# Kernel tuning notes

Hardware: AMD Instinct MI355X
Metric: run time of the kernel (lower is better)

## Reference

```python
import jax, jax.numpy as jnp
import numpy as np

B, C, H, W, D = 4, 8, 160, 160, 160
N_PER = 100000
IMAGE_DIM = 160


def setup_inputs() -> dict:
    key = jax.random.key(0)
    k1, k2 = jax.random.split(key)
    image_features = jax.random.normal(k1, (B, C, H, W, D), dtype=jnp.float32)
    # coords uniform in [0, IMAGE_DIM); last 3 columns are x,y,z
    graph_features = jax.random.uniform(k2, (B * N_PER, 3), dtype=jnp.float32) * IMAGE_DIM
    batch = jnp.arange(B * N_PER, dtype=jnp.int32) // N_PER  # equal count per image (required by cat dim=0)
    return {
        "image_features": image_features,
        "graph_features": graph_features,
        "batch": batch,
        "image_dim": IMAGE_DIM,
    }


def _trilerp(image_features, graph_features, image_dim):
    Bn, Cc, Hh, Ww, Dd = image_features.shape
    n_per = graph_features.shape[0] // Bn
    dt = graph_features.dtype
    factor = jnp.asarray(image_dim, dt) / Hh  # original uses image_dim/h for all axes
    xyz = graph_features[:, -3:].reshape(Bn, n_per, 3) / factor  # [B, n, 3]
    x, y, z = xyz[..., 0], xyz[..., 1], xyz[..., 2]

    def bounds(v, size):
        lo = jnp.minimum(jnp.floor(v), size - 1)
        hi = jnp.minimum(jnp.ceil(v), size - 1)
        return lo, hi

    x1f, x2f = bounds(x, Hh)
    y1f, y2f = bounds(y, Ww)
    z1f, z2f = bounds(z, Dd)
    x1, x2 = x1f.astype(jnp.int32), x2f.astype(jnp.int32)
    y1, y2 = y1f.astype(jnp.int32), y2f.astype(jnp.int32)
    z1, z2 = z1f.astype(jnp.int32), z2f.astype(jnp.int32)
    # weights exactly as in original (degenerate-to-zero when floor==ceil, kept faithfully)
    wx, wx2 = x - x1f, x2f - x
    wy, wy2 = y - y1f, y2f - y
    wz, wz2 = z - z1f, z2f - z

    def per_image(img, x1, x2, y1, y2, z1, z2, wx, wx2, wy, wy2, wz, wz2):
        # img: [C, H, W, D]; indices/weights: [n]
        def g(xi, yi, zi):
            return img[:, xi, yi, zi]  # [C, n]

        def lerp_y(zc):
            lx1 = g(x2, y1, zc) * wx + g(x1, y1, zc) * wx2
            lx2 = g(x2, y2, zc) * wx + g(x1, y2, zc) * wx2
            return lx2 * wy + lx1 * wy2

        return lerp_y(z2) * wz + lerp_y(z1) * wz2  # [C, n]

    out = jax.vmap(per_image)(
        image_features, x1, x2, y1, y2, z1, z2, wx, wx2, wy, wy2, wz, wz2
    )  # [B, C, n]
    # torch.cat over batch along dim 0 of [C, n] blocks == reshape to [B*C, n]; then permute(1,0)
    return out.reshape(Bn * Cc, n_per).T  # [n, B*C]


def reference(image_features, graph_features, batch, image_dim):
    # batch is arange(N)//n_per (sorted, equal counts), so grouping == reshape; batch unused numerically
    return _trilerp(image_features, graph_features, image_dim)
```

## Files before the change

kernel.cpp:

```cpp
#include <hip/hip_runtime.h>
#include <hip/hip_fp16.h>

constexpr int B = 4, C = 8, H = 160, W = 160, Dd = 160, NPER = 100000;
constexpr long HWD = (long)H * W * Dd;
constexpr int  TOTAL_PTS = NPER * B;
constexpr int  TOTAL_OUT = NPER * B * C;
constexpr int  NKEYS = B * H * W;
constexpr int  SCAN_BLOCKS = NKEYS / 256;

typedef float  f32x4 __attribute__((ext_vector_type(4)));

constexpr size_t WS_IMG_BYTES   = (size_t)B * HWD * C * sizeof(__half);
constexpr size_t WS_COUNTS_OFF  = WS_IMG_BYTES;
constexpr size_t WS_PART_OFF    = WS_COUNTS_OFF + (size_t)NKEYS * 4;
constexpr size_t WS_PAY_OFF     = WS_PART_OFF + 4096;
constexpr size_t WS_NEEDED      = WS_PAY_OFF + (size_t)TOTAL_PTS * 16;

__device__ __forceinline__ float load_image_dim(const int* dimp) {
    int iv = dimp[0];
    return (iv > 0 && iv < 1000000) ? (float)iv : __int_as_float(iv);
}

struct Coord {
    int x1, x2, y1, y2, z1, z2;
    float wx, wx2, wy, wy2, wz, wz2;
};
__device__ __forceinline__ Coord coord_from_xyz(float gx, float gy, float gz,
                                                float factor) {
    Coord c;
    float x = gx / factor, y = gy / factor, z = gz / factor;
    float x1f = fminf(floorf(x), (float)(H - 1));
    float x2f = fminf(ceilf(x),  (float)(H - 1));
    float y1f = fminf(floorf(y), (float)(W - 1));
    float y2f = fminf(ceilf(y),  (float)(W - 1));
    float z1f = fminf(floorf(z), (float)(Dd - 1));
    float z2f = fminf(ceilf(z),  (float)(Dd - 1));
    c.x1 = max(0, (int)x1f); c.x2 = max(0, (int)x2f);
    c.y1 = max(0, (int)y1f); c.y2 = max(0, (int)y2f);
    c.z1 = max(0, (int)z1f); c.z2 = max(0, (int)z2f);
    c.wx = x - x1f; c.wx2 = x2f - x;
    c.wy = y - y1f; c.wy2 = y2f - y;
    c.wz = z - z1f; c.wz2 = z2f - z;
    return c;
}

__global__ __launch_bounds__(256) void zero_kernel(int* __restrict__ counts) {
    int i = blockIdx.x * 256 + threadIdx.x;
    if (i < NKEYS) counts[i] = 0;
}

__global__ __launch_bounds__(256) void hist_kernel(
    const float* __restrict__ gf, const int* __restrict__ dimp,
    int* __restrict__ counts)
{
    int p = blockIdx.x * 256 + threadIdx.x;
    if (p >= TOTAL_PTS) return;
    float factor = load_image_dim(dimp) / (float)H;
    int b = p / NPER;
    Coord c = coord_from_xyz(gf[(long)p*3], gf[(long)p*3+1], gf[(long)p*3+2], factor);
    atomicAdd(&counts[(b * H + c.x1) * W + c.y1], 1);
}

__global__ __launch_bounds__(256) void scanA_kernel(
    int* __restrict__ counts, int* __restrict__ partials)
{
    __shared__ int sm[256];
    int g = blockIdx.x * 256 + threadIdx.x;
    int v = counts[g];
    sm[threadIdx.x] = v;
    __syncthreads();
    for (int off = 1; off < 256; off <<= 1) {
        int t = (threadIdx.x >= off) ? sm[threadIdx.x - off] : 0;
        __syncthreads();
        sm[threadIdx.x] += t;
        __syncthreads();
    }
    counts[g] = sm[threadIdx.x] - v;
    if (threadIdx.x == 255) partials[blockIdx.x] = sm[255];
}

__global__ __launch_bounds__(512) void scanB_kernel(int* __restrict__ partials)
{
    __shared__ int sm[512];
    int t = threadIdx.x;
    int v = (t < SCAN_BLOCKS) ? partials[t] : 0;
    sm[t] = v;
    __syncthreads();
    for (int off = 1; off < 512; off <<= 1) {
        int u = (t >= off) ? sm[t - off] : 0;
        __syncthreads();
        sm[t] += u;
        __syncthreads();
    }
    if (t < SCAN_BLOCKS) partials[t] = sm[t] - v;
}

__global__ __launch_bounds__(256) void scanC_kernel(
    int* __restrict__ counts, const int* __restrict__ partials)
{
    int g = blockIdx.x * 256 + threadIdx.x;
    counts[g] += partials[blockIdx.x];
}

__global__ __launch_bounds__(256) void scatter_kernel(
    const float* __restrict__ gf, const int* __restrict__ dimp,
    int* __restrict__ counts, f32x4* __restrict__ payload)
{
    int p = blockIdx.x * 256 + threadIdx.x;
    if (p >= TOTAL_PTS) return;
    float factor = load_image_dim(dimp) / (float)H;
    int b = p / NPER;
    float gx = gf[(long)p*3], gy = gf[(long)p*3+1], gz = gf[(long)p*3+2];
    Coord c = coord_from_xyz(gx, gy, gz, factor);
    int pos = atomicAdd(&counts[(b * H + c.x1) * W + c.y1], 1);
    f32x4 rec;
    rec.x = __int_as_float(p); rec.y = gx; rec.z = gy; rec.w = gz;
    payload[pos] = rec;
}

__global__ __launch_bounds__(256) void transpose_kernel(
    const float* __restrict__ img, __half* __restrict__ ws)
{
    long t = (long)blockIdx.x * 256 + threadIdx.x;
    const long nquads = (long)B * HWD / 4;
    if (t >= nquads) return;
    long v0 = t * 4;
    long b  = v0 / HWD;
    long v  = v0 - b * HWD;
    const float* base = img + b * C * HWD + v;

    f32x4 ch[8];
    #pragma unroll
    for (int c = 0; c < 8; ++c)
        ch[c] = __builtin_nontemporal_load(
            reinterpret_cast<const f32x4*>(base + (long)c * HWD));

    #pragma unroll
    for (int q = 0; q < 4; ++q) {
        __half h[8];
        #pragma unroll
        for (int c = 0; c < 8; ++c) h[c] = __float2half(ch[c][q]);
        *reinterpret_cast<f32x4*>(ws + (v0 + q) * 8) =
            *reinterpret_cast<const f32x4*>(h);
    }
}

__global__ __launch_bounds__(256) void gather_kernel(
    const __half* __restrict__ ws, const f32x4* __restrict__ payload,
    const int* __restrict__ dimp, float* __restrict__ out)
{
    int i = blockIdx.x * 256 + threadIdx.x;
    if (i >= TOTAL_PTS) return;
    f32x4 rec = payload[i];
    int p = __float_as_int(rec.x);
    int b = p / NPER;
    int j = p - b * NPER;

    float factor = load_image_dim(dimp) / (float)H;
    Coord cc = coord_from_xyz(rec.y, rec.z, rec.w, factor);

    const __half* base = ws + (long)b * HWD * 8;
    auto corner = [&](int xi, int yi, int zi, float* v) {
        long vox = ((long)xi * W + yi) * Dd + zi;
        f32x4 raw = *reinterpret_cast<const f32x4*>(base + vox * 8);
        const __half* h = reinterpret_cast<const __half*>(&raw);
        #pragma unroll
        for (int c = 0; c < 8; ++c) v[c] = __half2float(h[c]);
    };

    float a11[8], a12[8], a21[8], a22[8], ly_a[8], ly_b[8];

    corner(cc.x1, cc.y1, cc.z2, a11);
    corner(cc.x1, cc.y2, cc.z2, a12);
    corner(cc.x2, cc.y1, cc.z2, a21);
    corner(cc.x2, cc.y2, cc.z2, a22);
    #pragma unroll
    for (int c = 0; c < 8; ++c) {
        float lx1 = a21[c] * cc.wx + a11[c] * cc.wx2;
        float lx2 = a22[c] * cc.wx + a12[c] * cc.wx2;
        ly_a[c] = lx2 * cc.wy + lx1 * cc.wy2;
    }
    corner(cc.x1, cc.y1, cc.z1, a11);
    corner(cc.x1, cc.y2, cc.z1, a12);
    corner(cc.x2, cc.y1, cc.z1, a21);
    corner(cc.x2, cc.y2, cc.z1, a22);
    #pragma unroll
    for (int c = 0; c < 8; ++c) {
        float lx1 = a21[c] * cc.wx + a11[c] * cc.wx2;
        float lx2 = a22[c] * cc.wx + a12[c] * cc.wx2;
        ly_b[c] = lx2 * cc.wy + lx1 * cc.wy2;
    }

    f32x4 r0, r1;
    #pragma unroll
    for (int c = 0; c < 4; ++c) r0[c] = ly_a[c] * cc.wz + ly_b[c] * cc.wz2;
    #pragma unroll
    for (int c = 0; c < 4; ++c) r1[c] = ly_a[c+4] * cc.wz + ly_b[c+4] * cc.wz2;

    float* dst = out + (long)j * 32 + b * 8;
    __builtin_nontemporal_store(r0, reinterpret_cast<f32x4*>(dst));
    __builtin_nontemporal_store(r1, reinterpret_cast<f32x4*>(dst + 4));
}

__global__ __launch_bounds__(256) void og_proj_direct(
    const float* __restrict__ img, const float* __restrict__ gf,
    const int* __restrict__ dimp, float* __restrict__ out)
{
    int o = blockIdx.x * 256 + threadIdx.x;
    if (o >= TOTAL_OUT) return;
    int j = o >> 5, bc = o & 31, b = bc >> 3, c = bc & 7;
    float factor = load_image_dim(dimp) / (float)H;
    long p = (long)b * NPER + j;
    Coord cc = coord_from_xyz(gf[p*3], gf[p*3+1], gf[p*3+2], factor);

    const float* base = img + (size_t)(b * C + c) * (size_t)HWD;
    size_t r11 = ((size_t)cc.x1 * W + cc.y1) * Dd;
    size_t r12 = ((size_t)cc.x1 * W + cc.y2) * Dd;
    size_t r21 = ((size_t)cc.x2 * W + cc.y1) * Dd;
    size_t r22 = ((size_t)cc.x2 * W + cc.y2) * Dd;

    float lx1_a = base[r21 + cc.z2] * cc.wx + base[r11 + cc.z2] * cc.wx2;
    float lx2_a = base[r22 + cc.z2] * cc.wx + base[r12 + cc.z2] * cc.wx2;
    float ly_a  = lx2_a * cc.wy + lx1_a * cc.wy2;
    float lx1_b = base[r21 + cc.z1] * cc.wx + base[r11 + cc.z1] * cc.wx2;
    float lx2_b = base[r22 + cc.z1] * cc.wx + base[r12 + cc.z1] * cc.wx2;
    float ly_b  = lx2_b * cc.wy + lx1_b * cc.wy2;
    out[o] = ly_a * cc.wz + ly_b * cc.wz2;
}

extern "C" void kernel_launch(void* const* d_in, const int* in_sizes, int n_in,
                              void* d_out, int out_size, void* d_ws, size_t ws_size,
                              hipStream_t stream) {
    const float* img  = (const float*)d_in[0];
    const float* gf   = (const float*)d_in[1];
    const int*   dimp = (const int*)d_in[3];
    float* out = (float*)d_out;

    if (ws_size >= WS_NEEDED) {
        __half* ws   = (__half*)d_ws;
        int* counts  = (int*)((char*)d_ws + WS_COUNTS_OFF);
        int* parts   = (int*)((char*)d_ws + WS_PART_OFF);
        f32x4* payld = (f32x4*)((char*)d_ws + WS_PAY_OFF);

        int pblocks = (TOTAL_PTS + 255) / 256;
        zero_kernel<<<SCAN_BLOCKS, 256, 0, stream>>>(counts);
        hist_kernel<<<pblocks, 256, 0, stream>>>(gf, dimp, counts);
        scanA_kernel<<<SCAN_BLOCKS, 256, 0, stream>>>(counts, parts);
        scanB_kernel<<<1, 512, 0, stream>>>(parts);
        scanC_kernel<<<SCAN_BLOCKS, 256, 0, stream>>>(counts, parts);
        scatter_kernel<<<pblocks, 256, 0, stream>>>(gf, dimp, counts, payld);

        long nquads = (long)B * HWD / 4;
        int tblocks = (int)((nquads + 255) / 256);
        transpose_kernel<<<tblocks, 256, 0, stream>>>(img, ws);
        gather_kernel<<<pblocks, 256, 0, stream>>>(ws, payld, dimp, out);
    } else {
        int blocks = (TOTAL_OUT + 255) / 256;
        og_proj_direct<<<blocks, 256, 0, stream>>>(img, gf, dimp, out);
    }
}
```

Before: 230.4 us.

## Drop fp16 channel-interleaved transpose; gather directly from fp32 image per channel

Removes the pre-pass that converted the whole image to a channel-interleaved half-precision copy, and instead gathers the eight trilinear corners directly from the original fp32 planar image with one thread per point-channel pair. Blocks are remapped so contiguous ranges of spatially sorted points are scheduled on the same XCD to improve L2 locality. This avoids a full read and write of the large image volume, at the cost of more scattered narrow loads per point and eight times as many threads reading the payload.

```diff
diff --git a/kernel.cpp b/kernel.cpp
--- a/kernel.cpp
+++ b/kernel.cpp
@@ -1,5 +1,4 @@
 #include <hip/hip_runtime.h>
-#include <hip/hip_fp16.h>
 
 constexpr int B = 4, C = 8, H = 160, W = 160, Dd = 160, NPER = 100000;
 constexpr long HWD = (long)H * W * Dd;
@@ -8,13 +7,12 @@
 constexpr int  NKEYS = B * H * W;
 constexpr int  SCAN_BLOCKS = NKEYS / 256;
 
-typedef float  f32x4 __attribute__((ext_vector_type(4)));
-
-constexpr size_t WS_IMG_BYTES   = (size_t)B * HWD * C * sizeof(__half);
-constexpr size_t WS_COUNTS_OFF  = WS_IMG_BYTES;
-constexpr size_t WS_PART_OFF    = WS_COUNTS_OFF + (size_t)NKEYS * 4;
-constexpr size_t WS_PAY_OFF     = WS_PART_OFF + 4096;
-constexpr size_t WS_NEEDED      = WS_PAY_OFF + (size_t)TOTAL_PTS * 16;
+typedef float f32x4 __attribute__((ext_vector_type(4)));
+
+constexpr size_t WS_COUNTS_OFF = 0;
+constexpr size_t WS_PART_OFF   = (size_t)NKEYS * 4;
+constexpr size_t WS_PAY_OFF    = WS_PART_OFF + 4096;
+constexpr size_t WS_NEEDED     = WS_PAY_OFF + (size_t)TOTAL_PTS * 16;
 
 __device__ __forceinline__ float load_image_dim(const int* dimp) {
     int iv = dimp[0];
@@ -118,39 +116,19 @@
     payload[pos] = rec;
 }
 
-__global__ __launch_bounds__(256) void transpose_kernel(
-    const float* __restrict__ img, __half* __restrict__ ws)
-{
-    long t = (long)blockIdx.x * 256 + threadIdx.x;
-    const long nquads = (long)B * HWD / 4;
-    if (t >= nquads) return;
-    long v0 = t * 4;
-    long b  = v0 / HWD;
-    long v  = v0 - b * HWD;
-    const float* base = img + b * C * HWD + v;
-
-    f32x4 ch[8];
-    #pragma unroll
-    for (int c = 0; c < 8; ++c)
-        ch[c] = __builtin_nontemporal_load(
-            reinterpret_cast<const f32x4*>(base + (long)c * HWD));
-
-    #pragma unroll
-    for (int q = 0; q < 4; ++q) {
-        __half h[8];
-        #pragma unroll
-        for (int c = 0; c < 8; ++c) h[c] = __float2half(ch[c][q]);
-        *reinterpret_cast<f32x4*>(ws + (v0 + q) * 8) =
-            *reinterpret_cast<const f32x4*>(h);
-    }
-}
-
-__global__ __launch_bounds__(256) void gather_kernel(
-    const __half* __restrict__ ws, const f32x4* __restrict__ payload,
+__global__ __launch_bounds__(256) void gather_sorted(
+    const float* __restrict__ img, const f32x4* __restrict__ payload,
     const int* __restrict__ dimp, float* __restrict__ out)
 {
-    int i = blockIdx.x * 256 + threadIdx.x;
-    if (i >= TOTAL_PTS) return;
+    int nwg = gridDim.x;
+    int q = nwg >> 3, r = nwg & 7;
+    int xcd = blockIdx.x & 7, idx = blockIdx.x >> 3;
+    int wg = (xcd < r) ? xcd * (q + 1) + idx
+                       : r * (q + 1) + (xcd - r) * q + idx;
+    int t = wg * 256 + threadIdx.x;
+    if (t >= TOTAL_OUT) return;
+    int i = t >> 3, c = t & 7;
+
     f32x4 rec = payload[i];
     int p = __float_as_int(rec.x);
     int b = p / NPER;
@@ -159,47 +137,21 @@
     float factor = load_image_dim(dimp) / (float)H;
     Coord cc = coord_from_xyz(rec.y, rec.z, rec.w, factor);
 
-    const __half* base = ws + (long)b * HWD * 8;
-    auto corner = [&](int xi, int yi, int zi, float* v) {
-        long vox = ((long)xi * W + yi) * Dd + zi;
-        f32x4 raw = *reinterpret_cast<const f32x4*>(base + vox * 8);
-        const __half* h = reinterpret_cast<const __half*>(&raw);
-        #pragma unroll
-        for (int c = 0; c < 8; ++c) v[c] = __half2float(h[c]);
-    };
-
-    float a11[8], a12[8], a21[8], a22[8], ly_a[8], ly_b[8];
-
-    corner(cc.x1, cc.y1, cc.z2, a11);
-    corner(cc.x1, cc.y2, cc.z2, a12);
-    corner(cc.x2, cc.y1, cc.z2, a21);
-    corner(cc.x2, cc.y2, cc.z2, a22);
-    #pragma unroll
-    for (int c = 0; c < 8; ++c) {
-        float lx1 = a21[c] * cc.wx + a11[c] * cc.wx2;
-        float lx2 = a22[c] * cc.wx + a12[c] * cc.wx2;
-        ly_a[c] = lx2 * cc.wy + lx1 * cc.wy2;
-    }
-    corner(cc.x1, cc.y1, cc.z1, a11);
-    corner(cc.x1, cc.y2, cc.z1, a12);
-    corner(cc.x2, cc.y1, cc.z1, a21);
-    corner(cc.x2, cc.y2, cc.z1, a22);
-    #pragma unroll
-    for (int c = 0; c < 8; ++c) {
-        float lx1 = a21[c] * cc.wx + a11[c] * cc.wx2;
-        float lx2 = a22[c] * cc.wx + a12[c] * cc.wx2;
-        ly_b[c] = lx2 * cc.wy + lx1 * cc.wy2;
-    }
-
-    f32x4 r0, r1;
-    #pragma unroll
-    for (int c = 0; c < 4; ++c) r0[c] = ly_a[c] * cc.wz + ly_b[c] * cc.wz2;
-    #pragma unroll
-    for (int c = 0; c < 4; ++c) r1[c] = ly_a[c+4] * cc.wz + ly_b[c+4] * cc.wz2;
-
-    float* dst = out + (long)j * 32 + b * 8;
-    __builtin_nontemporal_store(r0, reinterpret_cast<f32x4*>(dst));
-    __builtin_nontemporal_store(r1, reinterpret_cast<f32x4*>(dst + 4));
+    const float* base = img + (long)(b * C + c) * HWD;
+    const float* r11 = base + ((long)cc.x1 * W + cc.y1) * Dd;
+    const float* r12 = base + ((long)cc.x1 * W + cc.y2) * Dd;
+    const float* r21 = base + ((long)cc.x2 * W + cc.y1) * Dd;
+    const float* r22 = base + ((long)cc.x2 * W + cc.y2) * Dd;
+
+    float lx1_a = r21[cc.z2] * cc.wx + r11[cc.z2] * cc.wx2;
+    float lx2_a = r22[cc.z2] * cc.wx + r12[cc.z2] * cc.wx2;
+    float ly_a  = lx2_a * cc.wy + lx1_a * cc.wy2;
+    float lx1_b = r21[cc.z1] * cc.wx + r11[cc.z1] * cc.wx2;
+    float lx2_b = r22[cc.z1] * cc.wx + r12[cc.z1] * cc.wx2;
+    float ly_b  = lx2_b * cc.wy + lx1_b * cc.wy2;
+    float res = ly_a * cc.wz + ly_b * cc.wz2;
+
+    __builtin_nontemporal_store(res, out + (long)j * 32 + b * 8 + c);
 }
 
 __global__ __launch_bounds__(256) void og_proj_direct(
@@ -237,10 +189,9 @@
     float* out = (float*)d_out;
 
     if (ws_size >= WS_NEEDED) {
-        __half* ws   = (__half*)d_ws;
-        int* counts  = (int*)((char*)d_ws + WS_COUNTS_OFF);
-        int* parts   = (int*)((char*)d_ws + WS_PART_OFF);
-        f32x4* payld = (f32x4*)((char*)d_ws + WS_PAY_OFF);
+        int*   counts = (int*)((char*)d_ws + WS_COUNTS_OFF);
+        int*   parts  = (int*)((char*)d_ws + WS_PART_OFF);
+        f32x4* payld  = (f32x4*)((char*)d_ws + WS_PAY_OFF);
 
         int pblocks = (TOTAL_PTS + 255) / 256;
         zero_kernel<<<SCAN_BLOCKS, 256, 0, stream>>>(counts);
@@ -250,10 +201,8 @@
         scanC_kernel<<<SCAN_BLOCKS, 256, 0, stream>>>(counts, parts);
         scatter_kernel<<<pblocks, 256, 0, stream>>>(gf, dimp, counts, payld);
 
-        long nquads = (long)B * HWD / 4;
-        int tblocks = (int)((nquads + 255) / 256);
-        transpose_kernel<<<tblocks, 256, 0, stream>>>(img, ws);
-        gather_kernel<<<pblocks, 256, 0, stream>>>(ws, payld, dimp, out);
+        int gblocks = (TOTAL_OUT + 255) / 256;
+        gather_sorted<<<gblocks, 256, 0, stream>>>(img, payld, dimp, out);
     } else {
         int blocks = (TOTAL_OUT + 255) / 256;
         og_proj_direct<<<blocks, 256, 0, stream>>>(img, gf, dimp, out);
```

After: 197.7 us. 1.17x faster.
